# Performance work log

Measured on AMD Instinct MI355X. Metric: run time of the kernel, lower is better.

The kernel has to match this reference:

```python
import jax, jax.numpy as jnp
import numpy as np

DIM = 768
NUM_HEADS = 16
D_K = DIM // NUM_HEADS


def setup_inputs() -> dict:
    key = jax.random.key(0)
    ks = jax.random.split(key, 9)
    B, T = 4, 2048
    s = 1.0 / np.sqrt(DIM)
    return {
        "x": jax.random.normal(ks[0], (B, T, DIM), dtype=jnp.float32),
        "Wq": jax.random.normal(ks[1], (DIM, DIM), dtype=jnp.float32) * s,
        "bq": jnp.zeros((DIM,), dtype=jnp.float32),
        "Wk": jax.random.normal(ks[2], (DIM, DIM), dtype=jnp.float32) * s,
        "bk": jnp.zeros((DIM,), dtype=jnp.float32),
        "Wv": jax.random.normal(ks[3], (DIM, DIM), dtype=jnp.float32) * s,
        "bv": jnp.zeros((DIM,), dtype=jnp.float32),
        "Wp": jax.random.normal(ks[4], (DIM, DIM), dtype=jnp.float32) * s,
        "bp": jnp.zeros((DIM,), dtype=jnp.float32),
    }


def reference(x, Wq, bq, Wk, bk, Wv, bv, Wp, bp):
    B, T, _ = x.shape
    # QKV projections (weights stored as [in, out])
    q = x @ Wq + bq
    k = x @ Wk + bk
    v = x @ Wv + bv
    # split heads: (B, H, T, d_k)
    q = q.reshape(B, T, NUM_HEADS, D_K).transpose(0, 2, 1, 3)
    k = k.reshape(B, T, NUM_HEADS, D_K).transpose(0, 2, 1, 3)
    v = v.reshape(B, T, NUM_HEADS, D_K).transpose(0, 2, 1, 3)
    # scaled dot-product attention; dropout omitted (eval mode)
    scores = jnp.einsum("bhtd,bhsd->bhts", q, k) / jnp.sqrt(jnp.float32(D_K))
    attn = jax.nn.softmax(scores, axis=-1)
    out = jnp.einsum("bhts,bhsd->bhtd", attn, v)
    out = out.transpose(0, 2, 1, 3).reshape(B, T, DIM)
    return out @ Wp + bp
```

## Files before the change

### kernel.cpp

```cpp
#include <hip/hip_runtime.h>
#include <math.h>

#define T_SEQ 2048
#define B_SZ  4
#define DIM   768
#define NH    16
#define DK    48
#define NQK   1536
#define N3    2304
#define LDP   72

typedef __bf16 bf16x8 __attribute__((ext_vector_type(8)));
typedef float  f32x4  __attribute__((ext_vector_type(4)));

__device__ __forceinline__ unsigned short f32_to_bf16(float f) {
    unsigned u = __float_as_uint(f);
    u += 0x7FFFu + ((u >> 16) & 1u);
    return (unsigned short)(u >> 16);
}
__device__ __forceinline__ unsigned pack_bf16x2(float a, float b) {
    return (unsigned)f32_to_bf16(a) | ((unsigned)f32_to_bf16(b) << 16);
}
__device__ __forceinline__ void lds_dma16(const unsigned short* g, unsigned short* l) {
    __builtin_amdgcn_global_load_lds(
        (const __attribute__((address_space(1))) unsigned int*)g,
        (__attribute__((address_space(3))) unsigned int*)l, 16, 0, 0);
}

__global__ __launch_bounds__(256) void cvt_x_kernel(
    const float* __restrict__ x, unsigned short* __restrict__ xb)
{
    int i = blockIdx.x * 256 + threadIdx.x;
    const float* p = x + (size_t)i * 8;
    float4 f0 = *(const float4*)p;
    float4 f1 = *(const float4*)(p + 4);
    uint4 u;
    u.x = pack_bf16x2(f0.x, f0.y);
    u.y = pack_bf16x2(f0.z, f0.w);
    u.z = pack_bf16x2(f1.x, f1.y);
    u.w = pack_bf16x2(f1.z, f1.w);
    *(uint4*)(xb + (size_t)i * 8) = u;
}

__global__ __launch_bounds__(256) void pack_w_kernel(
    const float* __restrict__ Wq, const float* __restrict__ Wk,
    const float* __restrict__ Wv, const float* __restrict__ Wp,
    unsigned short* __restrict__ Wt, unsigned short* __restrict__ Wpt,
    float qscale)
{
    __shared__ float T[32][33];
    const int mode = blockIdx.z;
    const float* W = (mode == 0) ? Wq : (mode == 1) ? Wk : (mode == 2) ? Wv : Wp;
    const float sc = (mode == 0) ? qscale : 1.0f;
    const int k0 = blockIdx.x * 32, c0 = blockIdx.y * 32;
    const int tx = threadIdx.x & 31, ty = threadIdx.x >> 5;

#pragma unroll
    for (int r = 0; r < 4; ++r) {
        int row = ty + r * 8;
        T[row][tx] = W[(size_t)(k0 + row) * DIM + c0 + tx];
    }
    __syncthreads();
#pragma unroll
    for (int r = 0; r < 4; ++r) {
        int j   = ty + r * 8;
        int col = c0 + j;
        int k   = k0 + tx;
        unsigned short v = f32_to_bf16(T[tx][j] * sc);
        if (mode < 3) Wt[(size_t)(mode * 768 + col) * DIM + k] = v;
        else          Wpt[(size_t)col * DIM + k] = v;
    }
}

__global__ __launch_bounds__(256) void pack_bias_kernel(
    const float* __restrict__ bq, const float* __restrict__ bk,
    const float* __restrict__ bv, float* __restrict__ b3, float qscale)
{
    int n = blockIdx.x * 256 + threadIdx.x;
    if (n >= N3) return;
    float v;
    if (n < 768)       v = bq[n] * qscale;
    else if (n < 1536) v = bk[n - 768];
    else               v = bv[n - 1536];
    b3[n] = v;
}

__global__ __launch_bounds__(256) void gemm_qkv_kernel(
    const unsigned short* __restrict__ A, const unsigned short* __restrict__ Bt,
    const float* __restrict__ bias, unsigned short* __restrict__ QK,
    unsigned short* __restrict__ vT)
{
    __shared__ unsigned short As[128 * 32];
    __shared__ unsigned short Bs[128 * 32];

    const int t = threadIdx.x;
    const int w = t >> 6, lane = t & 63, quad = lane >> 4, lr = lane & 15;
    const int wm = w >> 1, wn = w & 1;
    const int m0 = blockIdx.y * 128, n0 = blockIdx.x * 128;

    const int cw0 = w * 128, cw1 = w * 128 + 64;
    const int ca = cw0 + lane, cb = cw1 + lane;
    const int ra = ca >> 2, sa = (ca & 3) * 8;
    const int rb = cb >> 2, sb = (cb & 3) * 8;

    f32x4 acc[4][4] = {};

    for (int k0 = 0; k0 < DIM; k0 += 32) {
        __syncthreads();
        lds_dma16(A  + (size_t)(m0 + ra) * DIM + k0 + sa, As + cw0 * 8);
        lds_dma16(A  + (size_t)(m0 + rb) * DIM + k0 + sb, As + cw1 * 8);
        lds_dma16(Bt + (size_t)(n0 + ra) * DIM + k0 + sa, Bs + cw0 * 8);
        lds_dma16(Bt + (size_t)(n0 + rb) * DIM + k0 + sb, Bs + cw1 * 8);
        __syncthreads();

        bf16x8 af[4], bfr[4];
#pragma unroll
        for (int mt = 0; mt < 4; ++mt)
            af[mt] = *(const bf16x8*)&As[(wm * 64 + mt * 16 + lr) * 32 + quad * 8];
#pragma unroll
        for (int nt = 0; nt < 4; ++nt)
            bfr[nt] = *(const bf16x8*)&Bs[(wn * 64 + nt * 16 + lr) * 32 + quad * 8];
#pragma unroll
        for (int mt = 0; mt < 4; ++mt)
#pragma unroll
            for (int nt = 0; nt < 4; ++nt)
                acc[mt][nt] = __builtin_amdgcn_mfma_f32_16x16x32_bf16(
                    af[mt], bfr[nt], acc[mt][nt], 0, 0, 0);
    }

    if (blockIdx.x < 12) {
#pragma unroll
        for (int nt = 0; nt < 4; ++nt) {
            int col = n0 + wn * 64 + nt * 16 + lr;
            float bv = bias[col];
#pragma unroll
            for (int mt = 0; mt < 4; ++mt)
#pragma unroll
                for (int r = 0; r < 4; ++r) {
                    int row = m0 + wm * 64 + mt * 16 + quad * 4 + r;
                    QK[(size_t)row * NQK + col] = f32_to_bf16(acc[mt][nt][r] + bv);
                }
        }
    } else {
        const int bidx = m0 >> 11;
        const int ts_base = (m0 & 2047) + wm * 64;
#pragma unroll
        for (int nt = 0; nt < 4; ++nt) {
            int col = n0 + wn * 64 + nt * 16 + lr;
            int vcol = col - 1536;
            int hh = vcol / 48, cc = vcol - hh * 48;
            float bv = bias[col];
            unsigned short* dst0 = vT + ((size_t)(bidx * 16 + hh) * 48 + cc) * T_SEQ;
#pragma unroll
            for (int mt = 0; mt < 4; ++mt) {
                int ts = ts_base + mt * 16 + quad * 4;
                uint2 u;
                u.x = pack_bf16x2(acc[mt][nt][0] + bv, acc[mt][nt][1] + bv);
                u.y = pack_bf16x2(acc[mt][nt][2] + bv, acc[mt][nt][3] + bv);
                *(uint2*)(dst0 + ts) = u;
            }
        }
    }
}

__global__ __launch_bounds__(256) void gemm_out_kernel(
    const unsigned short* __restrict__ A, const unsigned short* __restrict__ Bt,
    const float* __restrict__ bias, float* __restrict__ C)
{
    __shared__ unsigned short As[128 * 32];
    __shared__ unsigned short Bs[128 * 32];

    const int t = threadIdx.x;
    const int w = t >> 6, lane = t & 63, quad = lane >> 4, lr = lane & 15;
    const int wm = w >> 1, wn = w & 1;
    const int m0 = blockIdx.y * 128, n0 = blockIdx.x * 128;

    const int cw0 = w * 128, cw1 = w * 128 + 64;
    const int ca = cw0 + lane, cb = cw1 + lane;
    const int ra = ca >> 2, sa = (ca & 3) * 8;
    const int rb = cb >> 2, sb = (cb & 3) * 8;

    f32x4 acc[4][4] = {};

    for (int k0 = 0; k0 < DIM; k0 += 32) {
        __syncthreads();
        lds_dma16(A  + (size_t)(m0 + ra) * DIM + k0 + sa, As + cw0 * 8);
        lds_dma16(A  + (size_t)(m0 + rb) * DIM + k0 + sb, As + cw1 * 8);
        lds_dma16(Bt + (size_t)(n0 + ra) * DIM + k0 + sa, Bs + cw0 * 8);
        lds_dma16(Bt + (size_t)(n0 + rb) * DIM + k0 + sb, Bs + cw1 * 8);
        __syncthreads();

        bf16x8 af[4], bfr[4];
#pragma unroll
        for (int mt = 0; mt < 4; ++mt)
            af[mt] = *(const bf16x8*)&As[(wm * 64 + mt * 16 + lr) * 32 + quad * 8];
#pragma unroll
        for (int nt = 0; nt < 4; ++nt)
            bfr[nt] = *(const bf16x8*)&Bs[(wn * 64 + nt * 16 + lr) * 32 + quad * 8];
#pragma unroll
        for (int mt = 0; mt < 4; ++mt)
#pragma unroll
            for (int nt = 0; nt < 4; ++nt)
                acc[mt][nt] = __builtin_amdgcn_mfma_f32_16x16x32_bf16(
                    af[mt], bfr[nt], acc[mt][nt], 0, 0, 0);
    }

#pragma unroll
    for (int nt = 0; nt < 4; ++nt) {
        int col = n0 + wn * 64 + nt * 16 + lr;
        float bv = bias[col];
#pragma unroll
        for (int mt = 0; mt < 4; ++mt)
#pragma unroll
            for (int r = 0; r < 4; ++r) {
                int row = m0 + wm * 64 + mt * 16 + quad * 4 + r;
                C[(size_t)row * DIM + col] = acc[mt][nt][r] + bv;
            }
    }
}

__global__ __launch_bounds__(256, 4) void attn_kernel(
    const unsigned short* __restrict__ QK, const unsigned short* __restrict__ vT,
    unsigned short* __restrict__ Ob)
{
    __shared__ unsigned short Ks[64 * 48];
    __shared__ unsigned short Vt[48 * 64];
    __shared__ unsigned short Ps[4 * 32 * LDP];
    __shared__ __align__(16) unsigned short Zs[8];

    const int t = threadIdx.x;
    const int w = t >> 6, lane = t & 63, quad = lane >> 4, lr = lane & 15;
    const int qt = blockIdx.x, h = blockIdx.y, b = blockIdx.z;
    const int base = b * T_SEQ, q0 = qt * 128;
    const int hq = h * DK, hk = 768 + h * DK;
    const int qrow = base + q0 + w * 32;

    if (t < 4) ((unsigned*)Zs)[t] = 0u;

    bf16x8 qa[2], qb[2];
#pragma unroll
    for (int mt = 0; mt < 2; ++mt) {
        const unsigned short* qp = QK + (size_t)(qrow + mt * 16 + lr) * NQK + hq;
        qa[mt] = *(const bf16x8*)(qp + quad * 8);
        qb[mt] = *(const bf16x8*)(qp + 32 + quad * 8);
    }

    const unsigned short* gp[3];
    unsigned short*       lp[3];
    int                   gstep[3];
#pragma unroll
    for (int i = 0; i < 3; ++i) {
        int c = w * 3 + i;
        if (c < 6) {
            int e = c * 512 + lane * 8;
            int r = e / 48, col = e - r * 48;
            gp[i]    = QK + (size_t)(base + r) * NQK + hk + col;
            lp[i]    = Ks + c * 512;
            gstep[i] = 64 * NQK;
        } else {
            int cc = c - 6;
            int e = cc * 512 + lane * 8;
            int d = e >> 6, key = e & 63;
            gp[i]    = vT + ((size_t)(b * NH + h) * DK + d) * T_SEQ + key;
            lp[i]    = Vt + cc * 512;
            gstep[i] = 64;
        }
    }

    f32x4 Oacc[2][3] = {};
    float l_acc[2] = {0.0f, 0.0f};
    unsigned short* Pw = Ps + (w * 32) * LDP;

    for (int kt = 0; kt < T_SEQ / 64; ++kt) {
        __syncthreads();
        lds_dma16(gp[0], lp[0]);
        lds_dma16(gp[1], lp[1]);
        lds_dma16(gp[2], lp[2]);
        gp[0] += gstep[0]; gp[1] += gstep[1]; gp[2] += gstep[2];
        __syncthreads();

        {
            bf16x8 ka[4], kb[4];
#pragma unroll
            for (int nt = 0; nt < 4; ++nt) {
                const unsigned short* kp = Ks + (nt * 16 + lr) * 48;
                ka[nt] = *(const bf16x8*)(kp + quad * 8);
                const unsigned short* kbp = (quad < 2) ? (kp + 32 + quad * 8) : Zs;
                kb[nt] = *(const bf16x8*)kbp;
            }
#pragma unroll
            for (int mt = 0; mt < 2; ++mt) {
                float rs = 0.0f;
#pragma unroll
                for (int nt = 0; nt < 4; ++nt) {
                    f32x4 st = {};
                    st = __builtin_amdgcn_mfma_f32_16x16x32_bf16(ka[nt], qa[mt], st, 0, 0, 0);
                    st = __builtin_amdgcn_mfma_f32_16x16x32_bf16(kb[nt], qb[mt], st, 0, 0, 0);
                    float p0 = __builtin_amdgcn_exp2f(st[0]);
                    float p1 = __builtin_amdgcn_exp2f(st[1]);
                    float p2 = __builtin_amdgcn_exp2f(st[2]);
                    float p3 = __builtin_amdgcn_exp2f(st[3]);
                    rs += (p0 + p1) + (p2 + p3);
                    uint2 pk;
                    pk.x = pack_bf16x2(p0, p1);
                    pk.y = pack_bf16x2(p2, p3);
                    *(uint2*)&Pw[(mt * 16 + lr) * LDP + nt * 16 + quad * 4] = pk;
                }
                rs += __shfl_xor(rs, 16);
                rs += __shfl_xor(rs, 32);
                l_acc[mt] += rs;
            }
        }

        {
            bf16x8 aP[2][2];
#pragma unroll
            for (int mt = 0; mt < 2; ++mt) {
                aP[mt][0] = *(const bf16x8*)&Pw[(mt * 16 + lr) * LDP + quad * 8];
                aP[mt][1] = *(const bf16x8*)&Pw[(mt * 16 + lr) * LDP + 32 + quad * 8];
            }
#pragma unroll
            for (int on = 0; on < 3; ++on) {
                const unsigned short* vp = Vt + (on * 16 + lr) * 64;
                bf16x8 v0 = *(const bf16x8*)(vp + quad * 8);
                bf16x8 v1 = *(const bf16x8*)(vp + 32 + quad * 8);
#pragma unroll
                for (int mt = 0; mt < 2; ++mt) {
                    Oacc[mt][on] = __builtin_amdgcn_mfma_f32_16x16x32_bf16(
                        aP[mt][0], v0, Oacc[mt][on], 0, 0, 0);
                    Oacc[mt][on] = __builtin_amdgcn_mfma_f32_16x16x32_bf16(
                        aP[mt][1], v1, Oacc[mt][on], 0, 0, 0);
                }
            }
        }
    }

#pragma unroll
    for (int mt = 0; mt < 2; ++mt) {
#pragma unroll
        for (int r = 0; r < 4; ++r) {
            float l = __shfl(l_acc[mt], quad * 4 + r);
            float inv = 1.0f / l;
            int row = qrow + mt * 16 + quad * 4 + r;
#pragma unroll
            for (int on = 0; on < 3; ++on)
                Ob[(size_t)row * DIM + h * DK + on * 16 + lr] =
                    f32_to_bf16(Oacc[mt][on][r] * inv);
        }
    }
}

extern "C" void kernel_launch(void* const* d_in, const int* in_sizes, int n_in,
                              void* d_out, int out_size, void* d_ws, size_t ws_size,
                              hipStream_t stream) {
    (void)in_sizes; (void)n_in; (void)out_size; (void)ws_size;

    const float* x  = (const float*)d_in[0];
    const float* Wq = (const float*)d_in[1];
    const float* bq = (const float*)d_in[2];
    const float* Wk = (const float*)d_in[3];
    const float* bk = (const float*)d_in[4];
    const float* Wv = (const float*)d_in[5];
    const float* bv = (const float*)d_in[6];
    const float* Wp = (const float*)d_in[7];
    const float* bp = (const float*)d_in[8];
    float* out = (float*)d_out;

    const size_t M = (size_t)B_SZ * T_SEQ;

    char* ws = (char*)d_ws;
    unsigned short* xb  = (unsigned short*)ws;  ws += M * DIM * 2;
    unsigned short* qk  = (unsigned short*)ws;  ws += M * NQK * 2;
    unsigned short* vT  = (unsigned short*)ws;  ws += M * DIM * 2;
    unsigned short* aob = (unsigned short*)ws;  ws += M * DIM * 2;
    unsigned short* Wt  = (unsigned short*)ws;  ws += (size_t)N3 * DIM * 2;
    unsigned short* Wpt = (unsigned short*)ws;  ws += (size_t)DIM * DIM * 2;
    float*          b3  = (float*)ws;           ws += N3 * 4;

    const float qscale = 0.14433756729740643f * 1.4426950408889634f;

    cvt_x_kernel<<<dim3((int)(M * DIM / 8 / 256)), 256, 0, stream>>>(x, xb);
    pack_w_kernel<<<dim3(DIM / 32, DIM / 32, 4), 256, 0, stream>>>(
        Wq, Wk, Wv, Wp, Wt, Wpt, qscale);
    pack_bias_kernel<<<dim3((N3 + 255) / 256), 256, 0, stream>>>(bq, bk, bv, b3, qscale);

    gemm_qkv_kernel<<<dim3(N3 / 128, (int)(M / 128)), 256, 0, stream>>>(
        xb, Wt, b3, qk, vT);

    attn_kernel<<<dim3(T_SEQ / 128, NH, B_SZ), 256, 0, stream>>>(qk, vT, aob);

    gemm_out_kernel<<<dim3(DIM / 128, (int)(M / 128)), 256, 0, stream>>>(
        aob, Wpt, bp, out);
}
```

Baseline: 274.9 us.

## Double-buffer LDS tiles in GEMMs and attention, swizzle P/V, use hardware bf16 pack

Both GEMM kernels and the attention kernel now use two LDS buffers, so the next tile's global-to-LDS DMA is issued before computing on the current tile, with a single barrier per iteration. This overlaps load latency with MFMA work. The attention P and V tiles switch from padded rows to an XOR-swizzled 64-wide layout to avoid bank conflicts, and the K zero-fill now uses register zeros instead of a shared zero buffer. bf16 packing uses the v_cvt_pk_bf16_f32 instruction. The extra LDS may reduce occupancy, and a single barrier while the DMA is in flight relies on the compiler's wait counters for correctness.

```diff
diff --git a/kernel.cpp b/kernel.cpp
--- a/kernel.cpp
+++ b/kernel.cpp
@@ -8,7 +8,6 @@
 #define DK    48
 #define NQK   1536
 #define N3    2304
-#define LDP   72
 
 typedef __bf16 bf16x8 __attribute__((ext_vector_type(8)));
 typedef float  f32x4  __attribute__((ext_vector_type(4)));
@@ -19,7 +18,9 @@
     return (unsigned short)(u >> 16);
 }
 __device__ __forceinline__ unsigned pack_bf16x2(float a, float b) {
-    return (unsigned)f32_to_bf16(a) | ((unsigned)f32_to_bf16(b) << 16);
+    unsigned r;
+    asm("v_cvt_pk_bf16_f32 %0, %1, %2" : "=v"(r) : "v"(a), "v"(b));
+    return r;
 }
 __device__ __forceinline__ void lds_dma16(const unsigned short* g, unsigned short* l) {
     __builtin_amdgcn_global_load_lds(
@@ -90,8 +91,8 @@
     const float* __restrict__ bias, unsigned short* __restrict__ QK,
     unsigned short* __restrict__ vT)
 {
-    __shared__ unsigned short As[128 * 32];
-    __shared__ unsigned short Bs[128 * 32];
+    __shared__ __align__(16) unsigned short As[2 * 128 * 32];
+    __shared__ __align__(16) unsigned short Bs[2 * 128 * 32];
 
     const int t = threadIdx.x;
     const int w = t >> 6, lane = t & 63, quad = lane >> 4, lr = lane & 15;
@@ -103,29 +104,44 @@
     const int ra = ca >> 2, sa = (ca & 3) * 8;
     const int rb = cb >> 2, sb = (cb & 3) * 8;
 
+    const unsigned short* Ara = A  + (size_t)(m0 + ra) * DIM + sa;
+    const unsigned short* Arb = A  + (size_t)(m0 + rb) * DIM + sb;
+    const unsigned short* Bra = Bt + (size_t)(n0 + ra) * DIM + sa;
+    const unsigned short* Brb = Bt + (size_t)(n0 + rb) * DIM + sb;
+
     f32x4 acc[4][4] = {};
 
+    lds_dma16(Ara, As + cw0 * 8);
+    lds_dma16(Arb, As + cw1 * 8);
+    lds_dma16(Bra, Bs + cw0 * 8);
+    lds_dma16(Brb, Bs + cw1 * 8);
+    __syncthreads();
+
     for (int k0 = 0; k0 < DIM; k0 += 32) {
-        __syncthreads();
-        lds_dma16(A  + (size_t)(m0 + ra) * DIM + k0 + sa, As + cw0 * 8);
-        lds_dma16(A  + (size_t)(m0 + rb) * DIM + k0 + sb, As + cw1 * 8);
-        lds_dma16(Bt + (size_t)(n0 + ra) * DIM + k0 + sa, Bs + cw0 * 8);
-        lds_dma16(Bt + (size_t)(n0 + rb) * DIM + k0 + sb, Bs + cw1 * 8);
-        __syncthreads();
+        const int cur = (k0 >> 5) & 1, nxt = cur ^ 1;
+        if (k0 + 32 < DIM) {
+            lds_dma16(Ara + k0 + 32, As + nxt * 4096 + cw0 * 8);
+            lds_dma16(Arb + k0 + 32, As + nxt * 4096 + cw1 * 8);
+            lds_dma16(Bra + k0 + 32, Bs + nxt * 4096 + cw0 * 8);
+            lds_dma16(Brb + k0 + 32, Bs + nxt * 4096 + cw1 * 8);
+        }
+        const unsigned short* Ac = As + cur * 4096;
+        const unsigned short* Bc = Bs + cur * 4096;
 
         bf16x8 af[4], bfr[4];
 #pragma unroll
         for (int mt = 0; mt < 4; ++mt)
-            af[mt] = *(const bf16x8*)&As[(wm * 64 + mt * 16 + lr) * 32 + quad * 8];
+            af[mt] = *(const bf16x8*)&Ac[(wm * 64 + mt * 16 + lr) * 32 + quad * 8];
 #pragma unroll
         for (int nt = 0; nt < 4; ++nt)
-            bfr[nt] = *(const bf16x8*)&Bs[(wn * 64 + nt * 16 + lr) * 32 + quad * 8];
+            bfr[nt] = *(const bf16x8*)&Bc[(wn * 64 + nt * 16 + lr) * 32 + quad * 8];
 #pragma unroll
         for (int mt = 0; mt < 4; ++mt)
 #pragma unroll
             for (int nt = 0; nt < 4; ++nt)
                 acc[mt][nt] = __builtin_amdgcn_mfma_f32_16x16x32_bf16(
                     af[mt], bfr[nt], acc[mt][nt], 0, 0, 0);
+        __syncthreads();
     }
 
     if (blockIdx.x < 12) {
@@ -167,8 +183,8 @@
     const unsigned short* __restrict__ A, const unsigned short* __restrict__ Bt,
     const float* __restrict__ bias, float* __restrict__ C)
 {
-    __shared__ unsigned short As[128 * 32];
-    __shared__ unsigned short Bs[128 * 32];
+    __shared__ __align__(16) unsigned short As[2 * 128 * 32];
+    __shared__ __align__(16) unsigned short Bs[2 * 128 * 32];
 
     const int t = threadIdx.x;
     const int w = t >> 6, lane = t & 63, quad = lane >> 4, lr = lane & 15;
@@ -180,29 +196,44 @@
     const int ra = ca >> 2, sa = (ca & 3) * 8;
     const int rb = cb >> 2, sb = (cb & 3) * 8;
 
+    const unsigned short* Ara = A  + (size_t)(m0 + ra) * DIM + sa;
+    const unsigned short* Arb = A  + (size_t)(m0 + rb) * DIM + sb;
+    const unsigned short* Bra = Bt + (size_t)(n0 + ra) * DIM + sa;
+    const unsigned short* Brb = Bt + (size_t)(n0 + rb) * DIM + sb;
+
     f32x4 acc[4][4] = {};
 
+    lds_dma16(Ara, As + cw0 * 8);
+    lds_dma16(Arb, As + cw1 * 8);
+    lds_dma16(Bra, Bs + cw0 * 8);
+    lds_dma16(Brb, Bs + cw1 * 8);
+    __syncthreads();
+
     for (int k0 = 0; k0 < DIM; k0 += 32) {
-        __syncthreads();
-        lds_dma16(A  + (size_t)(m0 + ra) * DIM + k0 + sa, As + cw0 * 8);
-        lds_dma16(A  + (size_t)(m0 + rb) * DIM + k0 + sb, As + cw1 * 8);
-        lds_dma16(Bt + (size_t)(n0 + ra) * DIM + k0 + sa, Bs + cw0 * 8);
-        lds_dma16(Bt + (size_t)(n0 + rb) * DIM + k0 + sb, Bs + cw1 * 8);
-        __syncthreads();
+        const int cur = (k0 >> 5) & 1, nxt = cur ^ 1;
+        if (k0 + 32 < DIM) {
+            lds_dma16(Ara + k0 + 32, As + nxt * 4096 + cw0 * 8);
+            lds_dma16(Arb + k0 + 32, As + nxt * 4096 + cw1 * 8);
+            lds_dma16(Bra + k0 + 32, Bs + nxt * 4096 + cw0 * 8);
+            lds_dma16(Brb + k0 + 32, Bs + nxt * 4096 + cw1 * 8);
+        }
+        const unsigned short* Ac = As + cur * 4096;
+        const unsigned short* Bc = Bs + cur * 4096;
 
         bf16x8 af[4], bfr[4];
 #pragma unroll
         for (int mt = 0; mt < 4; ++mt)
-            af[mt] = *(const bf16x8*)&As[(wm * 64 + mt * 16 + lr) * 32 + quad * 8];
+            af[mt] = *(const bf16x8*)&Ac[(wm * 64 + mt * 16 + lr) * 32 + quad * 8];
 #pragma unroll
         for (int nt = 0; nt < 4; ++nt)
-            bfr[nt] = *(const bf16x8*)&Bs[(wn * 64 + nt * 16 + lr) * 32 + quad * 8];
+            bfr[nt] = *(const bf16x8*)&Bc[(wn * 64 + nt * 16 + lr) * 32 + quad * 8];
 #pragma unroll
         for (int mt = 0; mt < 4; ++mt)
 #pragma unroll
             for (int nt = 0; nt < 4; ++nt)
                 acc[mt][nt] = __builtin_amdgcn_mfma_f32_16x16x32_bf16(
                     af[mt], bfr[nt], acc[mt][nt], 0, 0, 0);
+        __syncthreads();
     }
 
 #pragma unroll
@@ -223,10 +254,9 @@
     const unsigned short* __restrict__ QK, const unsigned short* __restrict__ vT,
     unsigned short* __restrict__ Ob)
 {
-    __shared__ unsigned short Ks[64 * 48];
-    __shared__ unsigned short Vt[48 * 64];
-    __shared__ unsigned short Ps[4 * 32 * LDP];
-    __shared__ __align__(16) unsigned short Zs[8];
+    __shared__ __align__(16) unsigned short Ks[2 * 64 * 48];
+    __shared__ __align__(16) unsigned short Vt[2 * 48 * 64];
+    __shared__ __align__(16) unsigned short Ps[4 * 32 * 64];
 
     const int t = threadIdx.x;
     const int w = t >> 6, lane = t & 63, quad = lane >> 4, lr = lane & 15;
@@ -234,8 +264,7 @@
     const int base = b * T_SEQ, q0 = qt * 128;
     const int hq = h * DK, hk = 768 + h * DK;
     const int qrow = base + q0 + w * 32;
-
-    if (t < 4) ((unsigned*)Zs)[t] = 0u;
+    const int psw = lr & 7;
 
     bf16x8 qa[2], qb[2];
 #pragma unroll
@@ -246,7 +275,7 @@
     }
 
     const unsigned short* gp[3];
-    unsigned short*       lp[3];
+    unsigned short*       lp0[3];
     int                   gstep[3];
 #pragma unroll
     for (int i = 0; i < 3; ++i) {
@@ -255,38 +284,51 @@
             int e = c * 512 + lane * 8;
             int r = e / 48, col = e - r * 48;
             gp[i]    = QK + (size_t)(base + r) * NQK + hk + col;
-            lp[i]    = Ks + c * 512;
+            lp0[i]   = Ks + c * 512;
             gstep[i] = 64 * NQK;
         } else {
             int cc = c - 6;
             int e = cc * 512 + lane * 8;
-            int d = e >> 6, key = e & 63;
+            int d = e >> 6, p = (e >> 3) & 7;
+            int key = (p ^ (d & 7)) * 8;
             gp[i]    = vT + ((size_t)(b * NH + h) * DK + d) * T_SEQ + key;
-            lp[i]    = Vt + cc * 512;
+            lp0[i]   = Vt + cc * 512;
             gstep[i] = 64;
         }
     }
+
+    lds_dma16(gp[0], lp0[0]); gp[0] += gstep[0];
+    lds_dma16(gp[1], lp0[1]); gp[1] += gstep[1];
+    lds_dma16(gp[2], lp0[2]); gp[2] += gstep[2];
+    __syncthreads();
 
     f32x4 Oacc[2][3] = {};
     float l_acc[2] = {0.0f, 0.0f};
-    unsigned short* Pw = Ps + (w * 32) * LDP;
+    unsigned short* Pw = Ps + (w * 32) * 64;
 
     for (int kt = 0; kt < T_SEQ / 64; ++kt) {
-        __syncthreads();
-        lds_dma16(gp[0], lp[0]);
-        lds_dma16(gp[1], lp[1]);
-        lds_dma16(gp[2], lp[2]);
-        gp[0] += gstep[0]; gp[1] += gstep[1]; gp[2] += gstep[2];
-        __syncthreads();
+        const int cur = kt & 1, nxt = cur ^ 1;
+        if (kt + 1 < T_SEQ / 64) {
+            lds_dma16(gp[0], lp0[0] + nxt * 3072); gp[0] += gstep[0];
+            lds_dma16(gp[1], lp0[1] + nxt * 3072); gp[1] += gstep[1];
+            lds_dma16(gp[2], lp0[2] + nxt * 3072); gp[2] += gstep[2];
+        }
+        const unsigned short* Kc = Ks + cur * 3072;
+        const unsigned short* Vc = Vt + cur * 3072;
 
         {
             bf16x8 ka[4], kb[4];
 #pragma unroll
-            for (int nt = 0; nt < 4; ++nt) {
-                const unsigned short* kp = Ks + (nt * 16 + lr) * 48;
-                ka[nt] = *(const bf16x8*)(kp + quad * 8);
-                const unsigned short* kbp = (quad < 2) ? (kp + 32 + quad * 8) : Zs;
-                kb[nt] = *(const bf16x8*)kbp;
+            for (int nt = 0; nt < 4; ++nt)
+                ka[nt] = *(const bf16x8*)(Kc + (nt * 16 + lr) * 48 + quad * 8);
+            if (quad < 2) {
+#pragma unroll
+                for (int nt = 0; nt < 4; ++nt)
+                    kb[nt] = *(const bf16x8*)(Kc + (nt * 16 + lr) * 48 + 32 + quad * 8);
+            } else {
+                bf16x8 z = {};
+#pragma unroll
+                for (int nt = 0; nt < 4; ++nt) kb[nt] = z;
             }
 #pragma unroll
             for (int mt = 0; mt < 2; ++mt) {
@@ -304,7 +346,9 @@
                     uint2 pk;
                     pk.x = pack_bf16x2(p0, p1);
                     pk.y = pack_bf16x2(p2, p3);
-                    *(uint2*)&Pw[(mt * 16 + lr) * LDP + nt * 16 + quad * 4] = pk;
+                    int eo = nt * 16 + quad * 4;
+                    int es = (((eo >> 3) ^ psw) << 3) | (eo & 7);
+                    *(uint2*)&Pw[(mt * 16 + lr) * 64 + es] = pk;
                 }
                 rs += __shfl_xor(rs, 16);
                 rs += __shfl_xor(rs, 32);
@@ -316,14 +360,14 @@
             bf16x8 aP[2][2];
 #pragma unroll
             for (int mt = 0; mt < 2; ++mt) {
-                aP[mt][0] = *(const bf16x8*)&Pw[(mt * 16 + lr) * LDP + quad * 8];
-                aP[mt][1] = *(const bf16x8*)&Pw[(mt * 16 + lr) * LDP + 32 + quad * 8];
+                aP[mt][0] = *(const bf16x8*)&Pw[(mt * 16 + lr) * 64 + ((quad ^ psw) * 8)];
+                aP[mt][1] = *(const bf16x8*)&Pw[(mt * 16 + lr) * 64 + (((4 + quad) ^ psw) * 8)];
             }
 #pragma unroll
             for (int on = 0; on < 3; ++on) {
-                const unsigned short* vp = Vt + (on * 16 + lr) * 64;
-                bf16x8 v0 = *(const bf16x8*)(vp + quad * 8);
-                bf16x8 v1 = *(const bf16x8*)(vp + 32 + quad * 8);
+                const unsigned short* vp = Vc + (on * 16 + lr) * 64;
+                bf16x8 v0 = *(const bf16x8*)(vp + ((quad ^ psw) * 8));
+                bf16x8 v1 = *(const bf16x8*)(vp + (((4 + quad) ^ psw) * 8));
 #pragma unroll
                 for (int mt = 0; mt < 2; ++mt) {
                     Oacc[mt][on] = __builtin_amdgcn_mfma_f32_16x16x32_bf16(
@@ -333,6 +377,7 @@
                 }
             }
         }
+        __syncthreads();
     }
 
 #pragma unroll
```

Measured after the change: 244.3 us. 1.13x faster.
